# Optimization experiments

Hardware: AMD Instinct MI355X
Metric: run time of the kernel (lower is better)

Reference implementation:

```python
import jax, jax.numpy as jnp
import numpy as np

B, T, D_MODEL = 2, 512, 1024
D_INNER, D_HEAD, D_CONV = 2048, 64, 4
N_HEADS, D_STATE = 32, 32
DT_MIN, DT_MAX, K_MAX, EPS = 1e-4, 0.1, 0.5, 1e-8


def setup_inputs():
    key = jax.random.key(0)
    ks = jax.random.split(key, 8)
    n = lambda k, sh, s=1.0: jax.random.normal(k, sh, jnp.float32) * s
    return {
        "x": n(ks[0], (B, T, D_MODEL)),
        "W_in": n(ks[1], (2 * D_INNER + N_HEADS * 2, D_MODEL), D_MODEL ** -0.5),
        "dw_weight": n(ks[2], (D_INNER, D_CONV), D_CONV ** -0.5),
        "dw_bias": n(ks[3], (D_INNER,), 0.1),
        "W_bc": n(ks[4], (N_HEADS * 4 * D_STATE, D_INNER), D_INNER ** -0.5),
        "W_out": n(ks[5], (D_MODEL, D_INNER), D_INNER ** -0.5),
        "skip": jnp.ones((D_INNER,), jnp.float32),
        "A_log": n(ks[6], (N_HEADS, D_STATE), 0.5),
        "dt_bias": n(ks[7], (N_HEADS,), 0.5),
    }


def _forward(x, W_in, dw_weight, dw_bias, W_bc, W_out, skip, A_log, dt_bias):
    Bsz, Tlen, D = x.shape
    DI, K = dw_weight.shape
    H, N = A_log.shape
    DH = DI // H
    # fused input projection: gate | value | per-token scan params (dt, damping)
    proj = jnp.einsum('btd,od->bto', x, W_in)
    gate = proj[..., :DI]
    value_raw = proj[..., DI:2 * DI]
    params = proj[..., 2 * DI:].reshape(Bsz, Tlen, H, 2)
    # causal depthwise conv1d (left-pad K-1 zeros == zero conv_state)
    xp = jnp.pad(value_raw, ((0, 0), (K - 1, 0), (0, 0)))
    conv = dw_bias + sum(xp[:, k:k + Tlen, :] * dw_weight[:, k] for k in range(K))
    value = jax.nn.silu(conv)  # (B,T,DI)
    # selective params
    dt = jnp.clip(jax.nn.softplus(params[..., 0] + dt_bias), DT_MIN, DT_MAX)  # (B,T,H)
    kd = K_MAX * jax.nn.sigmoid(params[..., 1])  # damping, (B,T,H)
    A = jnp.exp(A_log)  # (H,N) nonneg oscillator frequency^2
    # selective B/C: 4 blocks of d_state (Bz, Bx, Cz, Cx), L2-normalized over d_state
    bc = jnp.einsum('bti,oi->bto', value, W_bc).reshape(Bsz, Tlen, H, 4, N)
    bc = bc / (jnp.sqrt(jnp.sum(bc * bc, axis=-1, keepdims=True)) + EPS)
    Bz, Bx, Cz, Cx = bc[..., 0, :], bc[..., 1, :], bc[..., 2, :], bc[..., 3, :]
    u = value.reshape(Bsz, Tlen, H, DH)

    # implicit-method damped linear oscillatory SSM scan (LinOSS-IM):
    #   z_t = S*(z_{t-1} - dt*A*x_{t-1} + dt*Bz_t (x) u_t),  S = 1/(1 + dt*k + dt^2*A)
    #   x_t = x_{t-1} + dt*z_t + dt*Bx_t (x) u_t
    #   y_t = Cz_t . z_t + Cx_t . x_t
    def step(carry, inp):
        z, s = carry  # each (B,H,N,DH)
        u_t, dt_t, k_t, Bz_t, Bx_t, Cz_t, Cx_t = inp
        dtE = dt_t[:, :, None, None]
        S = 1.0 / (1.0 + dt_t[..., None] * k_t[..., None] + (dt_t * dt_t)[..., None] * A)  # (B,H,N)
        z = S[..., None] * (z - dtE * A[None, :, :, None] * s + dtE * (Bz_t[..., None] * u_t[:, :, None, :]))
        s = s + dtE * z + dtE * (Bx_t[..., None] * u_t[:, :, None, :])
        y = jnp.einsum('bhn,bhnd->bhd', Cz_t, z) + jnp.einsum('bhn,bhnd->bhd', Cx_t, s)
        return (z, s), y

    tm = lambda a: jnp.moveaxis(a, 1, 0)  # time-major for scan
    init = (jnp.zeros((Bsz, H, N, DH), x.dtype), jnp.zeros((Bsz, H, N, DH), x.dtype))
    _, ys = jax.lax.scan(step, init, (tm(u), tm(dt), tm(kd), tm(Bz), tm(Bx), tm(Cz), tm(Cx)))
    y = jnp.moveaxis(ys, 0, 1).reshape(Bsz, Tlen, DI)
    y = (y + skip * value) * jax.nn.silu(gate)
    return jnp.einsum('bti,oi->bto', y, W_out)


def reference(x, W_in, dw_weight, dw_bias, W_bc, W_out, skip, A_log, dt_bias):
    return _forward(x, W_in, dw_weight, dw_bias, W_bc, W_out, skip, A_log, dt_bias)
```

## Files before the change

### kernel.cpp

```cpp
#include <hip/hip_runtime.h>
#include <hip/hip_bf16.h>
#include <math.h>

#define BB 2
#define TT 512
#define DM 1024
#define DI 2048
#define DCONV 4
#define NH 32
#define NS 32
#define DH 64
#define PROJW 4160
#define BT (BB*TT)

typedef unsigned short u16;
typedef short bf16x8v __attribute__((ext_vector_type(8)));
typedef float f32x4 __attribute__((ext_vector_type(4)));
typedef u16 u16x4 __attribute__((ext_vector_type(4)));

__device__ __forceinline__ float sigmoidf_(float x) { return 1.0f / (1.0f + expf(-x)); }
__device__ __forceinline__ float siluf_(float x) { return x * sigmoidf_(x); }

struct HS { u16 h, s; };
__device__ __forceinline__ HS split1(float x) {
    HS r;
    unsigned u = __float_as_uint(x);
    unsigned rr = u + 0x7fffu + ((u >> 16) & 1u);
    r.h = (u16)(rr >> 16);
    float hf = __uint_as_float(((unsigned)r.h) << 16);
    float res = x - hf;
    unsigned u2 = __float_as_uint(res);
    unsigned r2 = u2 + 0x7fffu + ((u2 >> 16) & 1u);
    r.s = (u16)(r2 >> 16);
    return r;
}

__device__ __forceinline__ void async_copy16(const void* g, void* l) {
    __builtin_amdgcn_global_load_lds(
        (__attribute__((address_space(1))) void*)const_cast<void*>(g),
        (__attribute__((address_space(3))) void*)l,
        16, 0, 0);
}

__device__ __forceinline__ void async_copy4(const void* g, void* l) {
    __builtin_amdgcn_global_load_lds(
        (__attribute__((address_space(1))) void*)const_cast<void*>(g),
        (__attribute__((address_space(3))) void*)l,
        4, 0, 0);
}

__global__ __launch_bounds__(256) void split_kernel(const float* __restrict__ in,
                                                    u16* __restrict__ hi,
                                                    u16* __restrict__ lo,
                                                    int n4) {
    int i = blockIdx.x * 256 + threadIdx.x;
    if (i >= n4) return;
    float4 v = ((const float4*)in)[i];
    HS a = split1(v.x), b = split1(v.y), c = split1(v.z), d = split1(v.w);
    u16x4 h, s;
    h.x = a.h; h.y = b.h; h.z = c.h; h.w = d.h;
    s.x = a.s; s.y = b.s; s.z = c.s; s.w = d.s;
    ((u16x4*)hi)[i] = h;
    ((u16x4*)lo)[i] = s;
}

template<int BM, int BN, bool GUARD>
__global__ __launch_bounds__(256) void gemm_bf16x3(const u16* __restrict__ Ah,
                                                   const u16* __restrict__ Al,
                                                   const u16* __restrict__ Bh,
                                                   const u16* __restrict__ Bl,
                                                   float* __restrict__ C,
                                                   int M, int N, int K) {
    constexpr int MF = BM / 32;
    constexpr int NF = BN / 32;
    constexpr int ASEG = BM / 16, BSEG = BN / 16;
    constexpr int NSEG = 2 * ASEG + 2 * BSEG;
    constexpr int SEGW = NSEG / 4;

    __shared__ u16 lds[(2 * BM + 2 * BN) * 32];
    u16* Ah_s = lds;
    u16* Al_s = lds + BM * 32;
    u16* Bh_s = lds + 2 * BM * 32;
    u16* Bl_s = lds + (2 * BM + BN) * 32;

    const int tid = threadIdx.x;
    const int l = tid & 63;
    const int w = tid >> 6;
    const int wm = w >> 1, wn = w & 1;

    const int m0 = blockIdx.y * BM;
    const int n0 = blockIdx.x * BN;

    const u16* segg[SEGW];
    u16* segl[SEGW];
#pragma unroll
    for (int si = 0; si < SEGW; ++si) {
        int seg = w + si * 4;
        const u16* gmat;
        u16* lmat;
        int r0, rbase;
        if (seg < ASEG)                { gmat = Ah; lmat = Ah_s; r0 = seg * 16;                  rbase = m0; }
        else if (seg < 2 * ASEG)       { gmat = Al; lmat = Al_s; r0 = (seg - ASEG) * 16;         rbase = m0; }
        else if (seg < 2 * ASEG + BSEG){ gmat = Bh; lmat = Bh_s; r0 = (seg - 2 * ASEG) * 16;     rbase = n0; }
        else                           { gmat = Bl; lmat = Bl_s; r0 = (seg - 2 * ASEG - BSEG) * 16; rbase = n0; }
        segg[si] = gmat + (size_t)(rbase + r0 + (l >> 2)) * K + (l & 3) * 8;
        segl[si] = lmat + r0 * 32;
    }

    f32x4 acc[MF][NF];
#pragma unroll
    for (int i = 0; i < MF; ++i)
#pragma unroll
        for (int j = 0; j < NF; ++j) {
            f32x4 z = {0.0f, 0.0f, 0.0f, 0.0f};
            acc[i][j] = z;
        }

    const int lrow = l & 15;
    const int lko = (l >> 4) * 8;

    for (int k0 = 0; k0 < K; k0 += 32) {
#pragma unroll
        for (int si = 0; si < SEGW; ++si)
            async_copy16(segg[si] + k0, segl[si]);
        __syncthreads();

        bf16x8v af[MF][2], bfv[NF][2];
#pragma unroll
        for (int i = 0; i < MF; ++i) {
            int r = wm * (MF * 16) + i * 16 + lrow;
            af[i][0] = *(const bf16x8v*)&Ah_s[r * 32 + lko];
            af[i][1] = *(const bf16x8v*)&Al_s[r * 32 + lko];
        }
#pragma unroll
        for (int j = 0; j < NF; ++j) {
            int r = wn * (NF * 16) + j * 16 + lrow;
            bfv[j][0] = *(const bf16x8v*)&Bh_s[r * 32 + lko];
            bfv[j][1] = *(const bf16x8v*)&Bl_s[r * 32 + lko];
        }
#pragma unroll
        for (int i = 0; i < MF; ++i)
#pragma unroll
            for (int j = 0; j < NF; ++j) {
                acc[i][j] = __builtin_amdgcn_mfma_f32_16x16x32_bf16(af[i][0], bfv[j][0], acc[i][j], 0, 0, 0);
                acc[i][j] = __builtin_amdgcn_mfma_f32_16x16x32_bf16(af[i][0], bfv[j][1], acc[i][j], 0, 0, 0);
                acc[i][j] = __builtin_amdgcn_mfma_f32_16x16x32_bf16(af[i][1], bfv[j][0], acc[i][j], 0, 0, 0);
            }
        __syncthreads();
    }

#pragma unroll
    for (int i = 0; i < MF; ++i) {
        int mrow = m0 + wm * (MF * 16) + i * 16 + (l >> 4) * 4;
#pragma unroll
        for (int j = 0; j < NF; ++j) {
            int ncol = n0 + wn * (NF * 16) + j * 16 + lrow;
            if (!GUARD || ncol < N) {
#pragma unroll
                for (int r = 0; r < 4; ++r)
                    C[(size_t)(mrow + r) * N + ncol] = acc[i][j][r];
            }
        }
    }
}

__global__ __launch_bounds__(256) void conv_silu_kernel(const float* __restrict__ proj,
                                                        const float* __restrict__ dw_w,
                                                        const float* __restrict__ dw_b,
                                                        float* __restrict__ value,
                                                        u16* __restrict__ vh,
                                                        u16* __restrict__ vl) {
    int i = blockIdx.x * 256 + threadIdx.x;
    int dq = i & (DI / 4 - 1);
    int bt = i >> 9;
    int t = bt & (TT - 1);
    int di = dq * 4;
    const float* vr = proj + (size_t)bt * PROJW + DI + di;
    float4 zz = {0, 0, 0, 0};
    float4 x0 = (t >= 3) ? *(const float4*)(vr - 3 * PROJW) : zz;
    float4 x1 = (t >= 2) ? *(const float4*)(vr - 2 * PROJW) : zz;
    float4 x2 = (t >= 1) ? *(const float4*)(vr - 1 * PROJW) : zz;
    float4 x3 = *(const float4*)vr;
    float4 w0 = *(const float4*)&dw_w[(di + 0) * 4];
    float4 w1 = *(const float4*)&dw_w[(di + 1) * 4];
    float4 w2 = *(const float4*)&dw_w[(di + 2) * 4];
    float4 w3 = *(const float4*)&dw_w[(di + 3) * 4];
    float4 bb = *(const float4*)&dw_b[di];
    float4 v;
    v.x = siluf_(bb.x + x0.x * w0.x + x1.x * w0.y + x2.x * w0.z + x3.x * w0.w);
    v.y = siluf_(bb.y + x0.y * w1.x + x1.y * w1.y + x2.y * w1.z + x3.y * w1.w);
    v.z = siluf_(bb.z + x0.z * w2.x + x1.z * w2.y + x2.z * w2.z + x3.z * w2.w);
    v.w = siluf_(bb.w + x0.w * w3.x + x1.w * w3.y + x2.w * w3.z + x3.w * w3.w);
    ((float4*)value)[i] = v;
    HS a = split1(v.x), b = split1(v.y), c = split1(v.z), d = split1(v.w);
    u16x4 h, s;
    h.x = a.h; h.y = b.h; h.z = c.h; h.w = d.h;
    s.x = a.s; s.y = b.s; s.z = c.s; s.w = d.s;
    ((u16x4*)vh)[i] = h;
    ((u16x4*)vl)[i] = s;
}

__global__ __launch_bounds__(256) void dtkd_S_kernel(const float* __restrict__ proj,
                                                     const float* __restrict__ dt_bias,
                                                     const float* __restrict__ A_log,
                                                     float* __restrict__ dt_a,
                                                     float* __restrict__ S_a) {
    int idx = blockIdx.x * 256 + threadIdx.x;
    int n = idx & (NS - 1);
    int h = (idx >> 5) & (NH - 1);
    int bt = idx >> 10;
    const float* prow = proj + (size_t)bt * PROJW + 2 * DI;
    float p0 = prow[2 * h], p1 = prow[2 * h + 1];
    float xdt = p0 + dt_bias[h];
    float sp = fmaxf(xdt, 0.0f) + log1pf(expf(-fabsf(xdt)));
    float dt = fminf(fmaxf(sp, 1e-4f), 0.1f);
    float kd = 0.5f * sigmoidf_(p1);
    float A = expf(A_log[h * NS + n]);
    float S = 1.0f / (1.0f + dt * kd + dt * dt * A);
    S_a[idx] = S;
    if (n == 0) dt_a[bt * NH + h] = dt;
}

__global__ __launch_bounds__(256) void normalize_kernel(float* __restrict__ bc) {
    int idx = blockIdx.x * 256 + threadIdx.x;
    float v = bc[idx];
    float ss = v * v;
    ss += __shfl_xor(ss, 1);
    ss += __shfl_xor(ss, 2);
    ss += __shfl_xor(ss, 4);
    ss += __shfl_xor(ss, 8);
    ss += __shfl_xor(ss, 16);
    bc[idx] = v / (sqrtf(ss) + 1e-8f);
}

#define CH 64
#define NCH (TT / CH)

__global__ __launch_bounds__(256, 1) void scan_kernel(const float* __restrict__ value,
                                                      const float* __restrict__ bc,
                                                      const float* __restrict__ dt_a,
                                                      const float* __restrict__ S_a,
                                                      const float* __restrict__ A_log,
                                                      float* __restrict__ yout) {
    __shared__ float bcb[2][CH * 128];
    __shared__ float Sb [2][CH * 32];
    __shared__ float ub [2][CH * 64];
    __shared__ float dtb[2][4 * CH];

    const int bh = blockIdx.x;
    const int b = bh >> 5, h = bh & (NH - 1);
    const int tid = threadIdx.x;
    const int w = tid >> 6, l = tid & 63;
    const int dloc = l & 15;
    const int ng = l >> 4;
    const int n0 = ng * 8;
    const int r0 = w * 16;

    const float* bc0 = bc    + (size_t)b * TT * 4096 + h * 128;
    const float* S0  = S_a   + (size_t)b * TT * 1024 + h * 32;
    const float* u0  = value + (size_t)b * TT * DI   + h * DH;
    const float* dt0 = dt_a  + (size_t)b * TT * NH   + h;

    float a[8];
#pragma unroll
    for (int j = 0; j < 8; j++) a[j] = expf(A_log[h * NS + n0 + j]);

    float z[8], s[8];
#pragma unroll
    for (int j = 0; j < 8; j++) { z[j] = 0.0f; s[j] = 0.0f; }

    float* yp = yout + (size_t)b * TT * DI + h * DH + w * 16 + dloc;

    auto issue_chunk = [&](int t0, int bi) {
        {
            const float* src = bc0 + (size_t)(t0 + r0 + (l >> 5)) * 4096 + (l & 31) * 4;
            float* dst = &bcb[bi][r0 * 128];
#pragma unroll
            for (int i = 0; i < 8; ++i) {
                async_copy16(src, dst);
                src += 2 * 4096; dst += 2 * 128;
            }
        }
        {
            const float* src = S0 + (size_t)(t0 + r0 + (l >> 3)) * 1024 + (l & 7) * 4;
            float* dst = &Sb[bi][r0 * 32];
#pragma unroll
            for (int i = 0; i < 2; ++i) {
                async_copy16(src, dst);
                src += 8 * 1024; dst += 8 * 32;
            }
        }
        {
            const float* src = u0 + (size_t)(t0 + r0 + (l >> 4)) * DI + (l & 15) * 4;
            float* dst = &ub[bi][r0 * 64];
#pragma unroll
            for (int i = 0; i < 4; ++i) {
                async_copy16(src, dst);
                src += 4 * DI; dst += 4 * 64;
            }
        }
        {
            const float* src = dt0 + (size_t)(t0 + l) * NH;
            float* dst = &dtb[bi][w * CH];
            async_copy4(src, dst);
        }
    };

    issue_chunk(0, 0);

    for (int c = 0; c < NCH; ++c) {
        const int bi = c & 1;
        if (c + 1 < NCH) {
            issue_chunk((c + 1) * CH, bi ^ 1);
            asm volatile("s_waitcnt vmcnt(15)" ::: "memory");
        } else {
            asm volatile("s_waitcnt vmcnt(0)" ::: "memory");
        }
        __builtin_amdgcn_sched_barrier(0);
        __builtin_amdgcn_s_barrier();

#pragma unroll 2
        for (int r = 0; r < CH; ++r) {
            const float* bcr = &bcb[bi][r * 128];
            float bz[8], bx[8], cz[8], cx[8], Sv[8];
            *(float4*)&bz[0] = *(const float4*)&bcr[n0];
            *(float4*)&bz[4] = *(const float4*)&bcr[n0 + 4];
            *(float4*)&bx[0] = *(const float4*)&bcr[32 + n0];
            *(float4*)&bx[4] = *(const float4*)&bcr[32 + n0 + 4];
            *(float4*)&cz[0] = *(const float4*)&bcr[64 + n0];
            *(float4*)&cz[4] = *(const float4*)&bcr[64 + n0 + 4];
            *(float4*)&cx[0] = *(const float4*)&bcr[96 + n0];
            *(float4*)&cx[4] = *(const float4*)&bcr[96 + n0 + 4];
            const float* Sr = &Sb[bi][r * 32 + n0];
            *(float4*)&Sv[0] = *(const float4*)&Sr[0];
            *(float4*)&Sv[4] = *(const float4*)&Sr[4];
            float u_d = ub[bi][r * 64 + w * 16 + dloc];
            float dt = dtb[bi][w * CH + r];

            float dtu = dt * u_d;
            float y0 = 0.0f, y1 = 0.0f;
#pragma unroll
            for (int j = 0; j < 8; j++) {
                float dtA = dt * a[j];
                float t1v = fmaf(-dtA, s[j], z[j]);
                float t2v = fmaf(dtu, bz[j], t1v);
                float zn = Sv[j] * t2v;
                z[j] = zn;
                float sn = fmaf(dt, zn, fmaf(dtu, bx[j], s[j]));
                s[j] = sn;
                if (j & 1) { y1 = fmaf(cz[j], zn, y1); y1 = fmaf(cx[j], sn, y1); }
                else       { y0 = fmaf(cz[j], zn, y0); y0 = fmaf(cx[j], sn, y0); }
            }
            float y = y0 + y1;
            y += __shfl_xor(y, 16);
            y += __shfl_xor(y, 32);
            if (ng == 0) yp[(size_t)(c * CH + r) * DI] = y;
        }
        __builtin_amdgcn_s_barrier();
    }
}

__global__ __launch_bounds__(256) void fuse_kernel(const float* __restrict__ proj,
                                                   const float* __restrict__ value,
                                                   const float* __restrict__ skip,
                                                   const float* __restrict__ ysc,
                                                   u16* __restrict__ yh,
                                                   u16* __restrict__ yl) {
    int i = blockIdx.x * 256 + threadIdx.x;
    int dq = i & (DI / 4 - 1);
    int bt = i >> 9;
    int di = dq * 4;
    float4 g = *(const float4*)&proj[(size_t)bt * PROJW + di];
    float4 yv = ((const float4*)ysc)[i];
    float4 v = ((const float4*)value)[i];
    float4 sk = *(const float4*)&skip[di];
    float4 r;
    r.x = fmaf(sk.x, v.x, yv.x) * siluf_(g.x);
    r.y = fmaf(sk.y, v.y, yv.y) * siluf_(g.y);
    r.z = fmaf(sk.z, v.z, yv.z) * siluf_(g.z);
    r.w = fmaf(sk.w, v.w, yv.w) * siluf_(g.w);
    HS a = split1(r.x), b = split1(r.y), c = split1(r.z), d = split1(r.w);
    u16x4 h, s;
    h.x = a.h; h.y = b.h; h.z = c.h; h.w = d.h;
    s.x = a.s; s.y = b.s; s.z = c.s; s.w = d.s;
    ((u16x4*)yh)[i] = h;
    ((u16x4*)yl)[i] = s;
}

extern "C" void kernel_launch(void* const* d_in, const int* in_sizes, int n_in,
                              void* d_out, int out_size, void* d_ws, size_t ws_size,
                              hipStream_t stream) {
    const float* x       = (const float*)d_in[0];
    const float* W_in    = (const float*)d_in[1];
    const float* dw_w    = (const float*)d_in[2];
    const float* dw_b    = (const float*)d_in[3];
    const float* W_bc    = (const float*)d_in[4];
    const float* W_out   = (const float*)d_in[5];
    const float* skip    = (const float*)d_in[6];
    const float* A_log   = (const float*)d_in[7];
    const float* dt_bias = (const float*)d_in[8];
    float* out = (float*)d_out;

    float* ws    = (float*)d_ws;
    float* proj  = ws;
    float* value = proj  + (size_t)BT * PROJW;
    float* dt_a  = value + (size_t)BT * DI;
    float* S_a   = dt_a  + (size_t)BT * NH;
    float* bcw   = S_a   + (size_t)BT * NH * NS;
    float* ysc   = bcw   + (size_t)BT * 4096;
    u16* Aslot_h = (u16*)(ysc + (size_t)BT * DI);
    u16* Aslot_l = Aslot_h + 2097152;
    u16* Bslot_h = Aslot_l + 2097152;
    u16* Bslot_l = Bslot_h + 8388608;

    dim3 blk(256);

    split_kernel<<<dim3(1048576 / 4 / 256), blk, 0, stream>>>(x, Aslot_h, Aslot_l, 1048576 / 4);
    split_kernel<<<dim3(4259840 / 4 / 256), blk, 0, stream>>>(W_in, Bslot_h, Bslot_l, 4259840 / 4);

    gemm_bf16x3<64, 128, true><<<dim3(33, 16), blk, 0, stream>>>(
        Aslot_h, Aslot_l, Bslot_h, Bslot_l, proj, BT, PROJW, DM);

    conv_silu_kernel<<<dim3(BT * DI / 4 / 256), blk, 0, stream>>>(
        proj, dw_w, dw_b, value, Aslot_h, Aslot_l);

    dtkd_S_kernel<<<dim3(BT * NH * NS / 256), blk, 0, stream>>>(proj, dt_bias, A_log, dt_a, S_a);

    split_kernel<<<dim3(8388608 / 4 / 256), blk, 0, stream>>>(W_bc, Bslot_h, Bslot_l, 8388608 / 4);

    gemm_bf16x3<64, 128, false><<<dim3(32, 16), blk, 0, stream>>>(
        Aslot_h, Aslot_l, Bslot_h, Bslot_l, bcw, BT, 4096, DI);

    normalize_kernel<<<dim3(BT * 4096 / 256), blk, 0, stream>>>(bcw);

    scan_kernel<<<dim3(BB * NH), blk, 0, stream>>>(value, bcw, dt_a, S_a, A_log, ysc);

    fuse_kernel<<<dim3(BT * DI / 4 / 256), blk, 0, stream>>>(
        proj, value, skip, ysc, Aslot_h, Aslot_l);

    split_kernel<<<dim3(2097152 / 4 / 256), blk, 0, stream>>>(W_out, Bslot_h, Bslot_l, 2097152 / 4);

    gemm_bf16x3<64, 64, false><<<dim3(16, 16), blk, 0, stream>>>(
        Aslot_h, Aslot_l, Bslot_h, Bslot_l, out, BT, DM, DI);
}
```

Measured before the change: 457.1 us.

## Split scan over head-dim quarters with 4x more blocks and software-pipelined LDS loads

The scan kernel now launches four blocks per (batch, head), each covering 16 of the 64 head-dim columns. Each thread holds 2 state entries instead of 8, and the output reduction uses four shuffles across 16 lanes. The 64-block launch underfilled the GPU, and this split is meant to raise occupancy and shorten the per-thread serial dependency chain. Per-row shared-memory loads are software-pipelined two steps ahead. In exchange, the B/C/S chunks are reloaded redundantly by all four blocks, and the barrier and wait scheme now waits for all outstanding loads before issuing the next chunk.

```diff
diff --git a/kernel.cpp b/kernel.cpp
--- a/kernel.cpp
+++ b/kernel.cpp
@@ -236,6 +236,8 @@
 #define CH 64
 #define NCH (TT / CH)
 
+struct SReg2 { float bz[2], bx[2], cz[2], cx[2], S[2], u, dt; };
+
 __global__ __launch_bounds__(256, 1) void scan_kernel(const float* __restrict__ value,
                                                       const float* __restrict__ bc,
                                                       const float* __restrict__ dt_a,
@@ -244,37 +246,39 @@
                                                       float* __restrict__ yout) {
     __shared__ float bcb[2][CH * 128];
     __shared__ float Sb [2][CH * 32];
-    __shared__ float ub [2][CH * 64];
+    __shared__ float ub [2][CH * 16];
     __shared__ float dtb[2][4 * CH];
 
-    const int bh = blockIdx.x;
+    const int part = blockIdx.x >> 6;
+    const int bh = blockIdx.x & 63;
     const int b = bh >> 5, h = bh & (NH - 1);
     const int tid = threadIdx.x;
     const int w = tid >> 6, l = tid & 63;
-    const int dloc = l & 15;
-    const int ng = l >> 4;
-    const int n0 = ng * 8;
+    const int g = l & 15;
+    const int dl = w * 4 + (l >> 4);
+    const int d0 = part * 16;
+    const int n0 = 2 * g;
     const int r0 = w * 16;
 
     const float* bc0 = bc    + (size_t)b * TT * 4096 + h * 128;
     const float* S0  = S_a   + (size_t)b * TT * 1024 + h * 32;
-    const float* u0  = value + (size_t)b * TT * DI   + h * DH;
+    const float* u0  = value + (size_t)b * TT * DI   + h * DH + d0;
     const float* dt0 = dt_a  + (size_t)b * TT * NH   + h;
 
-    float a[8];
-#pragma unroll
-    for (int j = 0; j < 8; j++) a[j] = expf(A_log[h * NS + n0 + j]);
-
-    float z[8], s[8];
-#pragma unroll
-    for (int j = 0; j < 8; j++) { z[j] = 0.0f; s[j] = 0.0f; }
-
-    float* yp = yout + (size_t)b * TT * DI + h * DH + w * 16 + dloc;
-
-    auto issue_chunk = [&](int t0, int bi) {
+    float a[2];
+    a[0] = expf(A_log[h * NS + n0]);
+    a[1] = expf(A_log[h * NS + n0 + 1]);
+
+    float z[2] = {0.0f, 0.0f}, s[2] = {0.0f, 0.0f};
+
+    float* yp = yout + (size_t)b * TT * DI + h * DH + d0 + dl;
+
+    int bi = 0;
+
+    auto issue_chunk = [&](int t0, int dbuf) {
         {
             const float* src = bc0 + (size_t)(t0 + r0 + (l >> 5)) * 4096 + (l & 31) * 4;
-            float* dst = &bcb[bi][r0 * 128];
+            float* dst = &bcb[dbuf][r0 * 128];
 #pragma unroll
             for (int i = 0; i < 8; ++i) {
                 async_copy16(src, dst);
@@ -283,7 +287,7 @@
         }
         {
             const float* src = S0 + (size_t)(t0 + r0 + (l >> 3)) * 1024 + (l & 7) * 4;
-            float* dst = &Sb[bi][r0 * 32];
+            float* dst = &Sb[dbuf][r0 * 32];
 #pragma unroll
             for (int i = 0; i < 2; ++i) {
                 async_copy16(src, dst);
@@ -291,72 +295,66 @@
             }
         }
         {
-            const float* src = u0 + (size_t)(t0 + r0 + (l >> 4)) * DI + (l & 15) * 4;
-            float* dst = &ub[bi][r0 * 64];
-#pragma unroll
-            for (int i = 0; i < 4; ++i) {
-                async_copy16(src, dst);
-                src += 4 * DI; dst += 4 * 64;
-            }
+            const float* src = u0 + (size_t)(t0 + r0 + (l >> 2)) * DI + (l & 3) * 4;
+            async_copy16(src, &ub[dbuf][r0 * 16]);
         }
         {
             const float* src = dt0 + (size_t)(t0 + l) * NH;
-            float* dst = &dtb[bi][w * CH];
-            async_copy4(src, dst);
+            async_copy4(src, &dtb[dbuf][w * CH]);
         }
     };
 
+    auto ldr = [&](SReg2& rg, int r) {
+        const float* bcr = &bcb[bi][r * 128];
+        *(float2*)&rg.bz[0] = *(const float2*)&bcr[n0];
+        *(float2*)&rg.bx[0] = *(const float2*)&bcr[32 + n0];
+        *(float2*)&rg.cz[0] = *(const float2*)&bcr[64 + n0];
+        *(float2*)&rg.cx[0] = *(const float2*)&bcr[96 + n0];
+        *(float2*)&rg.S[0]  = *(const float2*)&Sb[bi][r * 32 + n0];
+        rg.u  = ub[bi][r * 16 + dl];
+        rg.dt = dtb[bi][w * CH + r];
+    };
+
+    auto stepc = [&](SReg2& rg) {
+        float dt = rg.dt;
+        float dtu = dt * rg.u;
+        float y = 0.0f;
+#pragma unroll
+        for (int j = 0; j < 2; ++j) {
+            float dtA = dt * a[j];
+            float t1v = fmaf(-dtA, s[j], z[j]);
+            float t2v = fmaf(dtu, rg.bz[j], t1v);
+            float zn = rg.S[j] * t2v;
+            z[j] = zn;
+            float sn = fmaf(dt, zn, fmaf(dtu, rg.bx[j], s[j]));
+            s[j] = sn;
+            y = fmaf(rg.cz[j], zn, y);
+            y = fmaf(rg.cx[j], sn, y);
+        }
+        y += __shfl_xor(y, 1);
+        y += __shfl_xor(y, 2);
+        y += __shfl_xor(y, 4);
+        y += __shfl_xor(y, 8);
+        if (g == 0) *yp = y;
+        yp += DI;
+    };
+
     issue_chunk(0, 0);
 
     for (int c = 0; c < NCH; ++c) {
-        const int bi = c & 1;
-        if (c + 1 < NCH) {
-            issue_chunk((c + 1) * CH, bi ^ 1);
-            asm volatile("s_waitcnt vmcnt(15)" ::: "memory");
-        } else {
-            asm volatile("s_waitcnt vmcnt(0)" ::: "memory");
-        }
-        __builtin_amdgcn_sched_barrier(0);
+        bi = c & 1;
+        asm volatile("s_waitcnt vmcnt(0)" ::: "memory");
         __builtin_amdgcn_s_barrier();
-
-#pragma unroll 2
-        for (int r = 0; r < CH; ++r) {
-            const float* bcr = &bcb[bi][r * 128];
-            float bz[8], bx[8], cz[8], cx[8], Sv[8];
-            *(float4*)&bz[0] = *(const float4*)&bcr[n0];
-            *(float4*)&bz[4] = *(const float4*)&bcr[n0 + 4];
-            *(float4*)&bx[0] = *(const float4*)&bcr[32 + n0];
-            *(float4*)&bx[4] = *(const float4*)&bcr[32 + n0 + 4];
-            *(float4*)&cz[0] = *(const float4*)&bcr[64 + n0];
-            *(float4*)&cz[4] = *(const float4*)&bcr[64 + n0 + 4];
-            *(float4*)&cx[0] = *(const float4*)&bcr[96 + n0];
-            *(float4*)&cx[4] = *(const float4*)&bcr[96 + n0 + 4];
-            const float* Sr = &Sb[bi][r * 32 + n0];
-            *(float4*)&Sv[0] = *(const float4*)&Sr[0];
-            *(float4*)&Sv[4] = *(const float4*)&Sr[4];
-            float u_d = ub[bi][r * 64 + w * 16 + dloc];
-            float dt = dtb[bi][w * CH + r];
-
-            float dtu = dt * u_d;
-            float y0 = 0.0f, y1 = 0.0f;
-#pragma unroll
-            for (int j = 0; j < 8; j++) {
-                float dtA = dt * a[j];
-                float t1v = fmaf(-dtA, s[j], z[j]);
-                float t2v = fmaf(dtu, bz[j], t1v);
-                float zn = Sv[j] * t2v;
-                z[j] = zn;
-                float sn = fmaf(dt, zn, fmaf(dtu, bx[j], s[j]));
-                s[j] = sn;
-                if (j & 1) { y1 = fmaf(cz[j], zn, y1); y1 = fmaf(cx[j], sn, y1); }
-                else       { y0 = fmaf(cz[j], zn, y0); y0 = fmaf(cx[j], sn, y0); }
-            }
-            float y = y0 + y1;
-            y += __shfl_xor(y, 16);
-            y += __shfl_xor(y, 32);
-            if (ng == 0) yp[(size_t)(c * CH + r) * DI] = y;
-        }
-        __builtin_amdgcn_s_barrier();
+        if (c + 1 < NCH) issue_chunk((c + 1) * CH, bi ^ 1);
+
+        SReg2 q0, q1, q2, q3;
+        ldr(q0, 0); ldr(q1, 1);
+        for (int p = 0; p < CH / 4; ++p) {
+            ldr(q2, 4 * p + 2);              stepc(q0);
+            ldr(q3, 4 * p + 3);              stepc(q1);
+            ldr(q0, (4 * p + 4) & (CH - 1)); stepc(q2);
+            ldr(q1, (4 * p + 5) & (CH - 1)); stepc(q3);
+        }
     }
 }
 
@@ -433,7 +431,7 @@
 
     normalize_kernel<<<dim3(BT * 4096 / 256), blk, 0, stream>>>(bcw);
 
-    scan_kernel<<<dim3(BB * NH), blk, 0, stream>>>(value, bcw, dt_a, S_a, A_log, ysc);
+    scan_kernel<<<dim3(4 * BB * NH), blk, 0, stream>>>(value, bcw, dt_a, S_a, A_log, ysc);
 
     fuse_kernel<<<dim3(BT * DI / 4 / 256), blk, 0, stream>>>(
         proj, value, skip, ysc, Aslot_h, Aslot_l);
```

After: 406.8 us. 11.0% less time.
